# Performance work log

Hardware: AMD Instinct MI355X
Metric: run time of the kernel (lower is better)

## Reference

```python
import jax, jax.numpy as jnp
import numpy as np

N = 100000
E = 1600000
IN_C, HID, HEADS, OUT_C = 128, 64, 4, 2
NEG_SLOPE = 0.2


def setup_inputs() -> dict:
    key = jax.random.key(0)
    ks = jax.random.split(key, 10)
    def glorot(k, shape):
        fan = shape[0] + shape[-1]
        return jax.random.uniform(k, shape, jnp.float32, -1.0, 1.0) * np.sqrt(6.0 / fan)
    x = jax.random.normal(ks[0], (N, IN_C), jnp.float32)
    edge_index = jax.random.randint(ks[1], (2, E), 0, N, jnp.int64)
    return {
        "x": x,
        "edge_index": edge_index,
        "W1": glorot(ks[2], (IN_C, HID)),
        "b1": jnp.zeros((HID,), jnp.float32),
        "W2": glorot(ks[3], (HID, HEADS * HID)),
        "att_src": glorot(ks[4], (HEADS, HID)) ,
        "att_dst": glorot(ks[5], (HEADS, HID)),
        "b2": jnp.zeros((HEADS * HID,), jnp.float32),
        "W3": glorot(ks[6], (HEADS * HID, OUT_C)),
        "b3": jnp.zeros((OUT_C,), jnp.float32),
    }


def _add_self_loops(edge_index, n):
    loop = jnp.arange(n, dtype=edge_index.dtype)
    src = jnp.concatenate([edge_index[0], loop])
    dst = jnp.concatenate([edge_index[1], loop])
    return src, dst


def gcn_conv(x, W, b, src, dst, n):
    # x' = X W, then symmetric deg-normalized scatter-add (self-loops included)
    xw = x @ W
    deg = jax.ops.segment_sum(jnp.ones_like(dst, dtype=xw.dtype), dst, num_segments=n)
    dinv = jnp.where(deg > 0, jax.lax.rsqrt(deg), 0.0)
    norm = dinv[src] * dinv[dst]                      # [E2]
    out = jax.ops.segment_sum(xw[src] * norm[:, None], dst, num_segments=n)
    return out + b


def gat_conv(x, W, att_src, att_dst, b, src, dst, n, heads, ch):
    xw = (x @ W).reshape(n, heads, ch)                # [N, H, C]
    a_s = (xw * att_src).sum(-1)                      # [N, H]
    a_d = (xw * att_dst).sum(-1)
    e = jax.nn.leaky_relu(a_s[src] + a_d[dst], NEG_SLOPE)   # [E2, H]
    # segment softmax over incoming edges per destination node
    m = jax.ops.segment_max(e, dst, num_segments=n)
    m = jnp.where(jnp.isfinite(m), m, 0.0)
    e = jnp.exp(e - m[dst])
    den = jax.ops.segment_sum(e, dst, num_segments=n)
    alpha = e / (den[dst] + 1e-16)                    # [E2, H]
    out = jax.ops.segment_sum(xw[src] * alpha[:, :, None], dst, num_segments=n)
    return out.reshape(n, heads * ch) + b


def reference(x, edge_index, W1, b1, W2, att_src, att_dst, b2, W3, b3):
    n = x.shape[0]
    src, dst = _add_self_loops(edge_index, n)
    h = jax.nn.relu(gcn_conv(x, W1, b1, src, dst, n))
    h = jax.nn.elu(gat_conv(h, W2, att_src, att_dst, b2, src, dst, n, HEADS, HID))
    return gcn_conv(h, W3, b3, src, dst, n)
```

## Files before the change

### kernel.cpp

```cpp
#include <hip/hip_runtime.h>
#include <math.h>

#define N_NODES 100000
#define N_EDGES 1600000
#define E2      (N_NODES + N_EDGES)
#define IN_C    128
#define HID     64
#define HEADS   4
#define HH      256
#define OUT_C   2
#define NEG_SLOPE 0.2f

#define SB   1024
#define NSB  ((N_NODES + SB - 1) / SB)
#define NRANGE 8
#define RDIV   12500
#define BINS   RDIV
#define NBK    100
#define CHUNK  (N_EDGES / NBK)
#define CITER  ((CHUNK + 255) / 256)
#define NHB    (NRANGE * NBK)
#define NFC    (N_EDGES / 256)
#define RT     10
#define NT1    6250
#define NGEMM1 ((NT1 + 3) / 4)

typedef __attribute__((ext_vector_type(8))) short bf16x8;
typedef __attribute__((ext_vector_type(4))) float f32x4;

__device__ __forceinline__ float bf2f(unsigned short u) {
    return __uint_as_float(((unsigned)u) << 16);
}
__device__ __forceinline__ unsigned short f2bf(float f) {
    unsigned u = __float_as_uint(f);
    u += 0x7fffu + ((u >> 16) & 1u);
    return (unsigned short)(u >> 16);
}


__global__ __launch_bounds__(256) void k_prep(const float* __restrict__ W2,
        const float* __restrict__ W1,
        const float* __restrict__ att_src, const float* __restrict__ att_dst,
        unsigned short* __restrict__ W2t, unsigned short* __restrict__ wsdt,
        unsigned short* __restrict__ W1t) {
    int b = blockIdx.x, t = threadIdx.x;
    if (b < 64) {
        int g = b * 256 + t;
        int k = g >> 8, n = g & 255;
        W2t[n * 64 + k] = f2bf(W2[g]);
        return;
    }
    if (b < 66) {
        int g = (b - 64) * 256 + t;
        wsdt[512 + g] = 0;
        int k = g >> 3, o = g & 7;
        int h = o & 3;
        const float* att = (o < 4) ? att_src : att_dst;
        float acc = 0.f;
        const float* wrow = W2 + (size_t)k * HH + h * 64;
        const float* arow = att + h * 64;
        for (int c = 0; c < 64; ++c) acc = fmaf(wrow[c], arow[c], acc);
        wsdt[o * 64 + k] = f2bf(acc);
        return;
    }
    int g = (b - 66) * 256 + t;
    int k = g >> 6, n = g & 63;
    W1t[n * 128 + k] = f2bf(W1[g]);
}

__global__ __launch_bounds__(256) void k_hista(const int* __restrict__ ei,
        unsigned short* __restrict__ hp16, unsigned short* __restrict__ rank16,
        const float* __restrict__ x, const unsigned short* __restrict__ W1t,
        unsigned short* __restrict__ xw1b) {
    __shared__ unsigned int hh[BINS];
    int b = blockIdx.x, t = threadIdx.x;
    if (b < NHB) {
        int r = b / NBK, k = b - r * NBK;
        for (int i = t; i < BINS; i += 256) hh[i] = 0u;
        __syncthreads();
        const int* dp = ei + N_EDGES + (size_t)k * CHUNK;
        unsigned short* rp = rank16 + (size_t)k * CHUNK;
        int lo = r * RDIV;
        for (int it = 0; it < CITER; ++it) {
            int idx = it * 256 + t;
            if (idx < CHUNK) {
                int d = dp[idx] - lo;
                if ((unsigned)d < (unsigned)RDIV) {
                    unsigned rk = atomicAdd(&hh[d], 1u);
                    rp[idx] = (unsigned short)rk;
                }
            }
        }
        __syncthreads();
        unsigned short* hp = hp16 + (size_t)b * BINS;
        for (int i = t; i < BINS; i += 256) hp[i] = (unsigned short)hh[i];
        return;
    }
    int lane = t & 63, wv = t >> 6;
    int m = lane & 15, quad = lane >> 4;
    bf16x8 B[4][4];
#pragma unroll
    for (int ct = 0; ct < 4; ++ct)
#pragma unroll
        for (int ks = 0; ks < 4; ++ks)
            B[ct][ks] = *(const bf16x8*)(W1t + (size_t)(ct * 16 + m) * IN_C
                                         + ks * 32 + quad * 8);
    int tile = (b - NHB) * 4 + wv;
    if (tile >= NT1) return;
    int rbase = tile * 16;
    const float* xp = x + (size_t)(rbase + m) * IN_C + quad * 8;
    f32x4 c0 = {0.f, 0.f, 0.f, 0.f}, c1 = c0, c2 = c0, c3 = c0;
#pragma unroll
    for (int ks = 0; ks < 4; ++ks) {
        float4 f0 = *(const float4*)(xp + ks * 32);
        float4 f1 = *(const float4*)(xp + ks * 32 + 4);
        bf16x8 a;
        a[0] = (short)f2bf(f0.x); a[1] = (short)f2bf(f0.y);
        a[2] = (short)f2bf(f0.z); a[3] = (short)f2bf(f0.w);
        a[4] = (short)f2bf(f1.x); a[5] = (short)f2bf(f1.y);
        a[6] = (short)f2bf(f1.z); a[7] = (short)f2bf(f1.w);
        c0 = __builtin_amdgcn_mfma_f32_16x16x32_bf16(a, B[0][ks], c0, 0, 0, 0);
        c1 = __builtin_amdgcn_mfma_f32_16x16x32_bf16(a, B[1][ks], c1, 0, 0, 0);
        c2 = __builtin_amdgcn_mfma_f32_16x16x32_bf16(a, B[2][ks], c2, 0, 0, 0);
        c3 = __builtin_amdgcn_mfma_f32_16x16x32_bf16(a, B[3][ks], c3, 0, 0, 0);
    }
    int row0 = rbase + quad * 4;
#pragma unroll
    for (int ct = 0; ct < 4; ++ct) {
        f32x4 c = (ct == 0) ? c0 : (ct == 1) ? c1 : (ct == 2) ? c2 : c3;
        unsigned short* p = xw1b + (size_t)row0 * HID + ct * 16 + m;
#pragma unroll
        for (int r = 0; r < 4; ++r) p[(size_t)r * HID] = f2bf(c[r]);
    }
}

__global__ __launch_bounds__(256) void k_scan1(unsigned short* __restrict__ hp16,
        int* __restrict__ cnt, int* __restrict__ bsum) {
    int b = blockIdx.x, t = threadIdx.x;
    int s = 0;
#pragma unroll
    for (int u = 0; u < 4; ++u) {
        int i = b * SB + u * 256 + t;
        if (i < N_NODES) {
            int r = i / RDIV, bin = i - r * RDIV;
            unsigned short* p = hp16 + (size_t)r * NBK * BINS + bin;
            unsigned acc = 0;
            for (int k = 0; k < NBK; ++k) {
                unsigned short hv = p[(size_t)k * BINS];
                p[(size_t)k * BINS] = (unsigned short)acc;
                acc += hv;
            }
            cnt[i] = (int)acc;
            s += (int)acc + 1;
        }
    }
#pragma unroll
    for (int off = 1; off < 64; off <<= 1) s += __shfl_xor(s, off);
    __shared__ int wsum[4];
    int lane = t & 63, wv = t >> 6;
    if (lane == 0) wsum[wv] = s;
    __syncthreads();
    if (t == 0) bsum[b] = (wsum[0] + wsum[1]) + (wsum[2] + wsum[3]);
}

__global__ __launch_bounds__(256) void k_scan3(const int* __restrict__ cnt,
        const int* __restrict__ bsum, int* __restrict__ rowptr,
        float* __restrict__ dinv, int* __restrict__ col) {
    int b = blockIdx.x, t = threadIdx.x;
    int lane = t & 63, wv = t >> 6;
    __shared__ int wred[4];
    {
        int v = (t < b) ? bsum[t] : 0;
#pragma unroll
        for (int off = 1; off < 64; off <<= 1) v += __shfl_xor(v, off);
        if (lane == 0) wred[wv] = v;
    }
    __syncthreads();
    int pre = (wred[0] + wred[1]) + (wred[2] + wred[3]);
    __syncthreads();

    int i = b * SB + t * 4;
    int c0 = 0, c1 = 0, c2 = 0, c3 = 0;
    if (i + 3 < N_NODES) {
        int4 v = *(const int4*)(cnt + i);
        c0 = v.x; c1 = v.y; c2 = v.z; c3 = v.w;
    } else if (i < N_NODES) {
        c0 = cnt[i];
        if (i + 1 < N_NODES) c1 = cnt[i + 1];
        if (i + 2 < N_NODES) c2 = cnt[i + 2];
    }
    int n0 = (i < N_NODES), n1 = (i + 1 < N_NODES),
        n2 = (i + 2 < N_NODES), n3 = (i + 3 < N_NODES);
    int d0 = c0 + n0, d1 = c1 + n1, d2 = c2 + n2, d3 = c3 + n3;
    int s = (d0 + d1) + (d2 + d3);
    int inc = s;
#pragma unroll
    for (int off = 1; off < 64; off <<= 1) {
        int u = __shfl_up(inc, off);
        if (lane >= off) inc += u;
    }
    __shared__ int wtot[4];
    if (lane == 63) wtot[wv] = inc;
    __syncthreads();
    int base = pre + (inc - s);
    for (int w = 0; w < wv; ++w) base += wtot[w];
    if (n0) { rowptr[i]     = base;                dinv[i]     = rsqrtf((float)d0); col[base] = i; }
    if (n1) { rowptr[i + 1] = base + d0;           dinv[i + 1] = rsqrtf((float)d1); col[base + d0] = i + 1; }
    if (n2) { rowptr[i + 2] = base + d0 + d1;      dinv[i + 2] = rsqrtf((float)d2); col[base + d0 + d1] = i + 2; }
    if (n3) { rowptr[i + 3] = base + d0 + d1 + d2; dinv[i + 3] = rsqrtf((float)d3); col[base + d0 + d1 + d2] = i + 3; }
    if (b == 0 && t == 0) rowptr[N_NODES] = E2;
}

__global__ void k_fill(const int* __restrict__ ei, const int* __restrict__ rowptr,
        const unsigned short* __restrict__ hp16,
        const unsigned short* __restrict__ rank16, int* __restrict__ col) {
    int b = blockIdx.x;
    int r = b / NFC;
    int c = b - r * NFC;
    int i = c * 256 + threadIdx.x;
    int d = ei[N_EDGES + i];
    int bin = d - r * RDIV;
    if ((unsigned)bin >= (unsigned)RDIV) return;
    int k = i / CHUNK;
    unsigned pos = (unsigned)rowptr[d] + 1u
                 + (unsigned)hp16[(size_t)(r * NBK + k) * BINS + bin]
                 + (unsigned)rank16[i];
    col[pos] = ei[i];
}

__global__ __launch_bounds__(256) void k_agg1(const int* __restrict__ rowptr,
        const int* __restrict__ col, const unsigned short* __restrict__ xw1b,
        const float* __restrict__ dinv, const float* __restrict__ b1,
        unsigned short* __restrict__ h1b) {
    int t = threadIdx.x;
    int lane = t & 63;
    int d = blockIdx.x * 4 + (t >> 6);
    if (d >= N_NODES) return;
    int start = rowptr[d], end = rowptr[d + 1];
    int sub = lane >> 4;
    int cpos = lane & 15;
    float4 acc = make_float4(0.f, 0.f, 0.f, 0.f);
    for (int base = start; base < end; base += 64) {
        int cnt = min(64, end - base);
        int sl = (base + lane < end) ? col[base + lane] : 0;
#pragma unroll 2
        for (int j = 0; j < cnt; j += 4) {
            int idx = j + sub;
            int sj = __shfl(sl, idx);
            if (idx < cnt) {
                float di = dinv[sj];
                ushort4 v = ((const ushort4*)(xw1b + (size_t)sj * HID))[cpos];
                acc.x = fmaf(di, bf2f(v.x), acc.x);
                acc.y = fmaf(di, bf2f(v.y), acc.y);
                acc.z = fmaf(di, bf2f(v.z), acc.z);
                acc.w = fmaf(di, bf2f(v.w), acc.w);
            }
        }
    }
    acc.x += __shfl_xor(acc.x, 16); acc.y += __shfl_xor(acc.y, 16);
    acc.z += __shfl_xor(acc.z, 16); acc.w += __shfl_xor(acc.w, 16);
    acc.x += __shfl_xor(acc.x, 32); acc.y += __shfl_xor(acc.y, 32);
    acc.z += __shfl_xor(acc.z, 32); acc.w += __shfl_xor(acc.w, 32);
    if (lane < 16) {
        float di = dinv[d];
        float4 b = ((const float4*)b1)[lane];
        float ox = fmaf(acc.x, di, b.x); ox = ox > 0.f ? ox : 0.f;
        float oy = fmaf(acc.y, di, b.y); oy = oy > 0.f ? oy : 0.f;
        float oz = fmaf(acc.z, di, b.z); oz = oz > 0.f ? oz : 0.f;
        float ow = fmaf(acc.w, di, b.w); ow = ow > 0.f ? ow : 0.f;
        ushort4 o = make_ushort4(f2bf(ox), f2bf(oy), f2bf(oz), f2bf(ow));
        ((ushort4*)(h1b + (size_t)d * HID))[lane] = o;
    }
}

__global__ __launch_bounds__(256) void k_attn(const unsigned short* __restrict__ h1b,
        const unsigned short* __restrict__ wsdt,
        float* __restrict__ a_s, float* __restrict__ a_d) {
    int t = threadIdx.x;
    int lane = t & 63, wv = t >> 6;
    int m = lane & 15, quad = lane >> 4;
    bf16x8 Bw0 = *(const bf16x8*)(wsdt + (size_t)m * 64 + quad * 8);
    bf16x8 Bw1 = *(const bf16x8*)(wsdt + (size_t)m * 64 + 32 + quad * 8);
    int tile = blockIdx.x * 4 + wv;
    if (tile >= NT1) return;
    int rbase = tile * 16;
    const unsigned short* ap = h1b + (size_t)(rbase + m) * 64 + quad * 8;
    bf16x8 a0 = *(const bf16x8*)(ap);
    bf16x8 a1 = *(const bf16x8*)(ap + 32);
    f32x4 aw = {0.f, 0.f, 0.f, 0.f};
    aw = __builtin_amdgcn_mfma_f32_16x16x32_bf16(a0, Bw0, aw, 0, 0, 0);
    aw = __builtin_amdgcn_mfma_f32_16x16x32_bf16(a1, Bw1, aw, 0, 0, 0);
    int row = rbase + quad * 4;
    if (m < 4) {
#pragma unroll
        for (int r = 0; r < 4; ++r) a_s[(row + r) * 4 + m] = aw[r];
    } else if (m < 8) {
#pragma unroll
        for (int r = 0; r < 4; ++r) a_d[(row + r) * 4 + (m - 4)] = aw[r];
    }
}

__global__ __launch_bounds__(256) void k_agg2u(const int* __restrict__ rowptr,
        const int* __restrict__ col, const unsigned short* __restrict__ h1b,
        const float* __restrict__ a_s, const float* __restrict__ a_d,
        unsigned short* __restrict__ ub, int dbase) {
    __shared__ int   ss[4][64];
    __shared__ float sp[4][64][4];
    int t = threadIdx.x;
    int lane = t & 63, wv = t >> 6;
    int d = dbase + blockIdx.x * 4 + wv;
    if (d >= N_NODES) return;
    const float4* as4 = (const float4*)a_s;
    float4 adv = ((const float4*)a_d)[d];
    int start = rowptr[d], end = rowptr[d + 1];

    float den0 = 0.f, den1 = 0.f, den2 = 0.f, den3 = 0.f;
    float acc0 = 0.f, acc1 = 0.f, acc2 = 0.f, acc3 = 0.f;
    for (int base = start; base < end; base += 64) {
        int cnt = min(64, end - base);
        float p0 = 0.f, p1 = 0.f, p2 = 0.f, p3 = 0.f;
        int s = 0;
        if (lane < cnt) {
            s = col[base + lane];
            float4 av = as4[s];
            float v;
            v = av.x + adv.x; v = v > 0.f ? v : NEG_SLOPE * v; p0 = __expf(v);
            v = av.y + adv.y; v = v > 0.f ? v : NEG_SLOPE * v; p1 = __expf(v);
            v = av.z + adv.z; v = v > 0.f ? v : NEG_SLOPE * v; p2 = __expf(v);
            v = av.w + adv.w; v = v > 0.f ? v : NEG_SLOPE * v; p3 = __expf(v);
            den0 += p0; den1 += p1; den2 += p2; den3 += p3;
        }
        ss[wv][lane] = s;
        ((float4*)sp[wv])[lane] = make_float4(p0, p1, p2, p3);
#pragma unroll 4
        for (int j = 0; j < cnt; ++j) {
            int sj = ss[wv][j];
            float4 pj = ((const float4*)sp[wv])[j];
            float v = bf2f(h1b[(unsigned)sj * 64u + (unsigned)lane]);
            acc0 = fmaf(pj.x, v, acc0);
            acc1 = fmaf(pj.y, v, acc1);
            acc2 = fmaf(pj.z, v, acc2);
            acc3 = fmaf(pj.w, v, acc3);
        }
    }
#pragma unroll
    for (int mk = 1; mk < 64; mk <<= 1) {
        den0 += __shfl_xor(den0, mk);
        den1 += __shfl_xor(den1, mk);
        den2 += __shfl_xor(den2, mk);
        den3 += __shfl_xor(den3, mk);
    }
    float u0 = acc0 / (den0 + 1e-16f);
    float u1 = acc1 / (den1 + 1e-16f);
    float u2 = acc2 / (den2 + 1e-16f);
    float u3 = acc3 / (den3 + 1e-16f);
    unsigned short* up = ub + (size_t)d * HH;
    up[lane]       = f2bf(u0);
    up[64 + lane]  = f2bf(u1);
    up[128 + lane] = f2bf(u2);
    up[192 + lane] = f2bf(u3);
}

__global__ __launch_bounds__(256) void k_gemm3m(const unsigned short* __restrict__ ub,
        const unsigned short* __restrict__ W2t, const float* __restrict__ b2,
        const float* __restrict__ W3, const float* __restrict__ dinv,
        float2* __restrict__ xw3) {
    int t = threadIdx.x;
    int lane = t & 63, wv = t >> 6;
    int m = lane & 15, quad = lane >> 4;
    int nb = wv * 64 + m;
    bf16x8 B[4][2];
#pragma unroll
    for (int ct = 0; ct < 4; ++ct)
#pragma unroll
        for (int ks = 0; ks < 2; ++ks)
            B[ct][ks] = *(const bf16x8*)(W2t + (size_t)(nb + ct * 16) * 64
                                         + ks * 32 + quad * 8);
    float bv[4]; float2 w3v[4];
#pragma unroll
    for (int ct = 0; ct < 4; ++ct) {
        int n = nb + ct * 16;
        bv[ct] = b2[n];
        w3v[ct] = ((const float2*)W3)[n];
    }
    __shared__ float red[4][16][2];
    int r0 = blockIdx.x * (RT * 16);
    for (int tile = 0; tile < RT; ++tile) {
        int rbase = r0 + tile * 16;
        const unsigned short* ap = ub + (size_t)(rbase + m) * HH + wv * 64 + quad * 8;
        bf16x8 a0 = *(const bf16x8*)(ap);
        bf16x8 a1 = *(const bf16x8*)(ap + 32);
        f32x4 c0 = {0.f, 0.f, 0.f, 0.f}, c1 = c0, c2 = c0, c3 = c0;
        c0 = __builtin_amdgcn_mfma_f32_16x16x32_bf16(a0, B[0][0], c0, 0, 0, 0);
        c1 = __builtin_amdgcn_mfma_f32_16x16x32_bf16(a0, B[1][0], c1, 0, 0, 0);
        c2 = __builtin_amdgcn_mfma_f32_16x16x32_bf16(a0, B[2][0], c2, 0, 0, 0);
        c3 = __builtin_amdgcn_mfma_f32_16x16x32_bf16(a0, B[3][0], c3, 0, 0, 0);
        c0 = __builtin_amdgcn_mfma_f32_16x16x32_bf16(a1, B[0][1], c0, 0, 0, 0);
        c1 = __builtin_amdgcn_mfma_f32_16x16x32_bf16(a1, B[1][1], c1, 0, 0, 0);
        c2 = __builtin_amdgcn_mfma_f32_16x16x32_bf16(a1, B[2][1], c2, 0, 0, 0);
        c3 = __builtin_amdgcn_mfma_f32_16x16x32_bf16(a1, B[3][1], c3, 0, 0, 0);
        float px[4] = {0.f, 0.f, 0.f, 0.f}, py[4] = {0.f, 0.f, 0.f, 0.f};
#pragma unroll
        for (int ct = 0; ct < 4; ++ct) {
            f32x4 c = (ct == 0) ? c0 : (ct == 1) ? c1 : (ct == 2) ? c2 : c3;
#pragma unroll
            for (int r = 0; r < 4; ++r) {
                float o = c[r] + bv[ct];
                o = o > 0.f ? o : expm1f(o);
                px[r] = fmaf(o, w3v[ct].x, px[r]);
                py[r] = fmaf(o, w3v[ct].y, py[r]);
            }
        }
#pragma unroll
        for (int mk = 1; mk < 16; mk <<= 1) {
#pragma unroll
            for (int r = 0; r < 4; ++r) {
                px[r] += __shfl_xor(px[r], mk);
                py[r] += __shfl_xor(py[r], mk);
            }
        }
        if (m == 0) {
#pragma unroll
            for (int r = 0; r < 4; ++r) {
                red[wv][quad * 4 + r][0] = px[r];
                red[wv][quad * 4 + r][1] = py[r];
            }
        }
        __syncthreads();
        if (t < 32) {
            int row = t >> 1, xy = t & 1;
            float s = red[0][row][xy] + red[1][row][xy]
                    + red[2][row][xy] + red[3][row][xy];
            ((float*)(xw3 + (rbase + row)))[xy] = s * dinv[rbase + row];
        }
        __syncthreads();
    }
}

__global__ __launch_bounds__(256) void k_agg3(const int* __restrict__ rowptr,
        const int* __restrict__ col, const float2* __restrict__ xw3,
        const float* __restrict__ dinv, const float* __restrict__ b3,
        float* __restrict__ out) {
    int t = threadIdx.x;
    int lane = t & 63;
    int g = lane >> 2, s = lane & 3;
    int d = blockIdx.x * 64 + (t >> 6) * 16 + g;
    if (d >= N_NODES) return;
    int e0 = rowptr[d], e1 = rowptr[d + 1];
    float a0 = 0.f, a1 = 0.f;
    for (int e = e0 + s; e < e1; e += 4) {
        float2 v = xw3[col[e]];
        a0 += v.x; a1 += v.y;
    }
    a0 += __shfl_xor(a0, 1); a1 += __shfl_xor(a1, 1);
    a0 += __shfl_xor(a0, 2); a1 += __shfl_xor(a1, 2);
    if (s == 0) {
        float di = dinv[d];
        out[d * 2 + 0] = fmaf(a0, di, b3[0]);
        out[d * 2 + 1] = fmaf(a1, di, b3[1]);
    }
}


extern "C" void kernel_launch(void* const* d_in, const int* in_sizes, int n_in,
                              void* d_out, int out_size, void* d_ws, size_t ws_size,
                              hipStream_t stream) {
    const float* x       = (const float*)d_in[0];
    const int*   ei      = (const int*)d_in[1];
    const float* W1      = (const float*)d_in[2];
    const float* b1      = (const float*)d_in[3];
    const float* W2      = (const float*)d_in[4];
    const float* att_src = (const float*)d_in[5];
    const float* att_dst = (const float*)d_in[6];
    const float* b2      = (const float*)d_in[7];
    const float* W3      = (const float*)d_in[8];
    const float* b3      = (const float*)d_in[9];
    float* out = (float*)d_out;
    (void)in_sizes; (void)n_in; (void)out_size; (void)ws_size;

    char* ws = (char*)d_ws;
    size_t off = 0;
    auto alloc = [&](size_t bytes) -> void* {
        void* p = ws + off;
        off = (off + bytes + 255) & ~(size_t)255;
        return p;
    };
    int*    rowptr = (int*)alloc((N_NODES + 1) * sizeof(int));
    int*    cnt    = (int*)alloc(N_NODES * sizeof(int));
    int*    bsum   = (int*)alloc(NSB * sizeof(int));
    int*    col    = (int*)alloc((size_t)E2 * sizeof(int));
    float*  dinv   = (float*)alloc(N_NODES * sizeof(float));
    unsigned short* W2t  = (unsigned short*)alloc(64 * 256 * sizeof(unsigned short));
    unsigned short* wsdt = (unsigned short*)alloc(16 * 64 * sizeof(unsigned short));
    unsigned short* W1t  = (unsigned short*)alloc(64 * 128 * sizeof(unsigned short));
    unsigned short* xw1b = (unsigned short*)alloc((size_t)N_NODES * HID * sizeof(unsigned short));
    unsigned short* h1b  = (unsigned short*)alloc((size_t)N_NODES * HID * sizeof(unsigned short));
    float*  a_s    = (float*)alloc((size_t)N_NODES * HEADS * sizeof(float));
    float*  a_d    = (float*)alloc((size_t)N_NODES * HEADS * sizeof(float));
    unsigned short* ub   = (unsigned short*)alloc((size_t)N_NODES * HH * sizeof(unsigned short));
    float2* xw3    = (float2*)alloc((size_t)N_NODES * sizeof(float2));
    unsigned short* hp16   = ub;
    unsigned short* rank16 = ub + (size_t)NHB * BINS;

    k_prep<<<98, 256, 0, stream>>>(W2, W1, att_src, att_dst, W2t, wsdt, W1t);
    k_hista<<<NHB + NGEMM1, 256, 0, stream>>>(ei, hp16, rank16, x, W1t, xw1b);
    k_scan1<<<NSB, 256, 0, stream>>>(hp16, cnt, bsum);
    k_scan3<<<NSB, 256, 0, stream>>>(cnt, bsum, rowptr, dinv, col);
    k_fill<<<NRANGE * NFC, 256, 0, stream>>>(ei, rowptr, hp16, rank16, col);

    k_agg1<<<(N_NODES + 3) / 4, 256, 0, stream>>>(rowptr, col, xw1b, dinv, b1, h1b);
    k_attn<<<(NT1 + 3) / 4, 256, 0, stream>>>(h1b, wsdt, a_s, a_d);
    const int HALF = 50000;
    k_agg2u<<<HALF / 4, 256, 0, stream>>>(rowptr, col, h1b, a_s, a_d, ub, 0);
    k_agg2u<<<(N_NODES - HALF + 3) / 4, 256, 0, stream>>>(rowptr, col, h1b, a_s, a_d, ub, HALF);
    k_gemm3m<<<(N_NODES / 16) / RT, 256, 0, stream>>>(ub, W2t, b2, W3, dinv, xw3);
    k_agg3<<<(N_NODES + 63) / 64, 256, 0, stream>>>(rowptr, col, xw3, dinv, b3, out);
}
```

Baseline: 400.9 us.

## Move layer-1 GEMM from histogram kernel into fill kernel; vectorize histogram loads

The bf16 MFMA GEMM for X·W1 is moved out of the histogram kernel and into the edge-fill kernel as extra leading blocks. The histogram kernel now reads destination indices as int4, and its block index is remapped so the 8 range blocks sharing a chunk run next to each other for cache reuse. The aim is to balance work between the launches and cut load instructions in the histogram pass. In exchange, the GEMM now overlaps with the scattered fill stores instead of with the LDS atomics.

After: 398.0 us. No clear change (-0.7%).

```diff
diff --git a/kernel.cpp b/kernel.cpp
--- a/kernel.cpp
+++ b/kernel.cpp
@@ -18,7 +18,8 @@
 #define BINS   RDIV
 #define NBK    100
 #define CHUNK  (N_EDGES / NBK)
-#define CITER  ((CHUNK + 255) / 256)
+#define C4     (CHUNK / 4)
+#define CITER4 ((C4 + 255) / 256)
 #define NHB    (NRANGE * NBK)
 #define NFC    (N_EDGES / 256)
 #define RT     10
@@ -68,70 +69,36 @@
     W1t[n * 128 + k] = f2bf(W1[g]);
 }
 
-__global__ __launch_bounds__(256) void k_hista(const int* __restrict__ ei,
-        unsigned short* __restrict__ hp16, unsigned short* __restrict__ rank16,
-        const float* __restrict__ x, const unsigned short* __restrict__ W1t,
-        unsigned short* __restrict__ xw1b) {
+__global__ __launch_bounds__(256) void k_hist(const int* __restrict__ ei,
+        unsigned short* __restrict__ hp16, unsigned short* __restrict__ rank16) {
     __shared__ unsigned int hh[BINS];
     int b = blockIdx.x, t = threadIdx.x;
-    if (b < NHB) {
-        int r = b / NBK, k = b - r * NBK;
-        for (int i = t; i < BINS; i += 256) hh[i] = 0u;
-        __syncthreads();
-        const int* dp = ei + N_EDGES + (size_t)k * CHUNK;
-        unsigned short* rp = rank16 + (size_t)k * CHUNK;
-        int lo = r * RDIV;
-        for (int it = 0; it < CITER; ++it) {
-            int idx = it * 256 + t;
-            if (idx < CHUNK) {
-                int d = dp[idx] - lo;
-                if ((unsigned)d < (unsigned)RDIV) {
-                    unsigned rk = atomicAdd(&hh[d], 1u);
-                    rp[idx] = (unsigned short)rk;
-                }
-            }
-        }
-        __syncthreads();
-        unsigned short* hp = hp16 + (size_t)b * BINS;
-        for (int i = t; i < BINS; i += 256) hp[i] = (unsigned short)hh[i];
-        return;
-    }
-    int lane = t & 63, wv = t >> 6;
-    int m = lane & 15, quad = lane >> 4;
-    bf16x8 B[4][4];
-#pragma unroll
-    for (int ct = 0; ct < 4; ++ct)
-#pragma unroll
-        for (int ks = 0; ks < 4; ++ks)
-            B[ct][ks] = *(const bf16x8*)(W1t + (size_t)(ct * 16 + m) * IN_C
-                                         + ks * 32 + quad * 8);
-    int tile = (b - NHB) * 4 + wv;
-    if (tile >= NT1) return;
-    int rbase = tile * 16;
-    const float* xp = x + (size_t)(rbase + m) * IN_C + quad * 8;
-    f32x4 c0 = {0.f, 0.f, 0.f, 0.f}, c1 = c0, c2 = c0, c3 = c0;
-#pragma unroll
-    for (int ks = 0; ks < 4; ++ks) {
-        float4 f0 = *(const float4*)(xp + ks * 32);
-        float4 f1 = *(const float4*)(xp + ks * 32 + 4);
-        bf16x8 a;
-        a[0] = (short)f2bf(f0.x); a[1] = (short)f2bf(f0.y);
-        a[2] = (short)f2bf(f0.z); a[3] = (short)f2bf(f0.w);
-        a[4] = (short)f2bf(f1.x); a[5] = (short)f2bf(f1.y);
-        a[6] = (short)f2bf(f1.z); a[7] = (short)f2bf(f1.w);
-        c0 = __builtin_amdgcn_mfma_f32_16x16x32_bf16(a, B[0][ks], c0, 0, 0, 0);
-        c1 = __builtin_amdgcn_mfma_f32_16x16x32_bf16(a, B[1][ks], c1, 0, 0, 0);
-        c2 = __builtin_amdgcn_mfma_f32_16x16x32_bf16(a, B[2][ks], c2, 0, 0, 0);
-        c3 = __builtin_amdgcn_mfma_f32_16x16x32_bf16(a, B[3][ks], c3, 0, 0, 0);
-    }
-    int row0 = rbase + quad * 4;
-#pragma unroll
-    for (int ct = 0; ct < 4; ++ct) {
-        f32x4 c = (ct == 0) ? c0 : (ct == 1) ? c1 : (ct == 2) ? c2 : c3;
-        unsigned short* p = xw1b + (size_t)row0 * HID + ct * 16 + m;
-#pragma unroll
-        for (int r = 0; r < 4; ++r) p[(size_t)r * HID] = f2bf(c[r]);
-    }
+    int r = b & 7, k = b >> 3;
+    for (int i = t; i < BINS; i += 256) hh[i] = 0u;
+    __syncthreads();
+    const int4* dp4 = (const int4*)(ei + N_EDGES + (size_t)k * CHUNK);
+    unsigned short* rp = rank16 + (size_t)k * CHUNK;
+    int lo = r * RDIV;
+#pragma unroll 2
+    for (int it = 0; it < CITER4; ++it) {
+        int i4 = it * 256 + t;
+        if (i4 < C4) {
+            int4 v = dp4[i4];
+            int base = i4 * 4;
+            int d0 = v.x - lo, d1 = v.y - lo, d2 = v.z - lo, d3 = v.w - lo;
+            if ((unsigned)d0 < (unsigned)RDIV)
+                rp[base + 0] = (unsigned short)atomicAdd(&hh[d0], 1u);
+            if ((unsigned)d1 < (unsigned)RDIV)
+                rp[base + 1] = (unsigned short)atomicAdd(&hh[d1], 1u);
+            if ((unsigned)d2 < (unsigned)RDIV)
+                rp[base + 2] = (unsigned short)atomicAdd(&hh[d2], 1u);
+            if ((unsigned)d3 < (unsigned)RDIV)
+                rp[base + 3] = (unsigned short)atomicAdd(&hh[d3], 1u);
+        }
+    }
+    __syncthreads();
+    unsigned short* hp = hp16 + (size_t)(r * NBK + k) * BINS;
+    for (int i = t; i < BINS; i += 256) hp[i] = (unsigned short)hh[i];
 }
 
 __global__ __launch_bounds__(256) void k_scan1(unsigned short* __restrict__ hp16,
@@ -211,13 +178,55 @@
     if (b == 0 && t == 0) rowptr[N_NODES] = E2;
 }
 
-__global__ void k_fill(const int* __restrict__ ei, const int* __restrict__ rowptr,
-        const unsigned short* __restrict__ hp16,
-        const unsigned short* __restrict__ rank16, int* __restrict__ col) {
-    int b = blockIdx.x;
-    int r = b / NFC;
-    int c = b - r * NFC;
-    int i = c * 256 + threadIdx.x;
+__global__ __launch_bounds__(256) void k_fillg(const int* __restrict__ ei,
+        const int* __restrict__ rowptr, const unsigned short* __restrict__ hp16,
+        const unsigned short* __restrict__ rank16, int* __restrict__ col,
+        const float* __restrict__ x, const unsigned short* __restrict__ W1t,
+        unsigned short* __restrict__ xw1b) {
+    int b = blockIdx.x, t = threadIdx.x;
+    if (b < NGEMM1) {
+        int lane = t & 63, wv = t >> 6;
+        int m = lane & 15, quad = lane >> 4;
+        bf16x8 B[4][4];
+#pragma unroll
+        for (int ct = 0; ct < 4; ++ct)
+#pragma unroll
+            for (int ks = 0; ks < 4; ++ks)
+                B[ct][ks] = *(const bf16x8*)(W1t + (size_t)(ct * 16 + m) * IN_C
+                                             + ks * 32 + quad * 8);
+        int tile = b * 4 + wv;
+        if (tile >= NT1) return;
+        int rbase = tile * 16;
+        const float* xp = x + (size_t)(rbase + m) * IN_C + quad * 8;
+        f32x4 c0 = {0.f, 0.f, 0.f, 0.f}, c1 = c0, c2 = c0, c3 = c0;
+#pragma unroll
+        for (int ks = 0; ks < 4; ++ks) {
+            float4 f0 = *(const float4*)(xp + ks * 32);
+            float4 f1 = *(const float4*)(xp + ks * 32 + 4);
+            bf16x8 a;
+            a[0] = (short)f2bf(f0.x); a[1] = (short)f2bf(f0.y);
+            a[2] = (short)f2bf(f0.z); a[3] = (short)f2bf(f0.w);
+            a[4] = (short)f2bf(f1.x); a[5] = (short)f2bf(f1.y);
+            a[6] = (short)f2bf(f1.z); a[7] = (short)f2bf(f1.w);
+            c0 = __builtin_amdgcn_mfma_f32_16x16x32_bf16(a, B[0][ks], c0, 0, 0, 0);
+            c1 = __builtin_amdgcn_mfma_f32_16x16x32_bf16(a, B[1][ks], c1, 0, 0, 0);
+            c2 = __builtin_amdgcn_mfma_f32_16x16x32_bf16(a, B[2][ks], c2, 0, 0, 0);
+            c3 = __builtin_amdgcn_mfma_f32_16x16x32_bf16(a, B[3][ks], c3, 0, 0, 0);
+        }
+        int row0 = rbase + quad * 4;
+#pragma unroll
+        for (int ct = 0; ct < 4; ++ct) {
+            f32x4 c = (ct == 0) ? c0 : (ct == 1) ? c1 : (ct == 2) ? c2 : c3;
+            unsigned short* p = xw1b + (size_t)row0 * HID + ct * 16 + m;
+#pragma unroll
+            for (int r = 0; r < 4; ++r) p[(size_t)r * HID] = f2bf(c[r]);
+        }
+        return;
+    }
+    int bb = b - NGEMM1;
+    int r = bb / NFC;
+    int c = bb - r * NFC;
+    int i = c * 256 + t;
     int d = ei[N_EDGES + i];
     int bin = d - r * RDIV;
     if ((unsigned)bin >= (unsigned)RDIV) return;
@@ -503,10 +512,11 @@
     unsigned short* rank16 = ub + (size_t)NHB * BINS;
 
     k_prep<<<98, 256, 0, stream>>>(W2, W1, att_src, att_dst, W2t, wsdt, W1t);
-    k_hista<<<NHB + NGEMM1, 256, 0, stream>>>(ei, hp16, rank16, x, W1t, xw1b);
+    k_hist<<<NHB, 256, 0, stream>>>(ei, hp16, rank16);
     k_scan1<<<NSB, 256, 0, stream>>>(hp16, cnt, bsum);
     k_scan3<<<NSB, 256, 0, stream>>>(cnt, bsum, rowptr, dinv, col);
-    k_fill<<<NRANGE * NFC, 256, 0, stream>>>(ei, rowptr, hp16, rank16, col);
+    k_fillg<<<NGEMM1 + NRANGE * NFC, 256, 0, stream>>>(ei, rowptr, hp16, rank16,
+                                                       col, x, W1t, xw1b);
 
     k_agg1<<<(N_NODES + 3) / 4, 256, 0, stream>>>(rowptr, col, xw1b, dinv, b1, h1b);
     k_attn<<<(NT1 + 3) / 4, 256, 0, stream>>>(h1b, wsdt, a_s, a_d);
```
